# Kernel optimization log

Measured on AMD Instinct MI355X. Metric: run time of the kernel, lower is better.

## Reference

```python
import jax, jax.numpy as jnp
import numpy as np

B, H, W = 8, 64, 64
DIM1, DIM2 = 384, 256
NH, DH = 8, 32
INNER = NH * DH
EPS = 1e-5


def _layernorm(x, w, b):
    mu = jnp.mean(x, axis=-1, keepdims=True)
    var = jnp.mean((x - mu) ** 2, axis=-1, keepdims=True)
    return (x - mu) * jax.lax.rsqrt(var + EPS) * w + b


def _axial_attn(q, k, v, scale):
    # q,k,v: [B,H,W,nh,dh]; row attention over H, col attention over W
    sh = jnp.einsum('biwnd,bjwnd->bwnij', q, k) * scale  # [B,W,nh,H,H]
    oh = jnp.einsum('bwnij,bjwnd->biwnd', jax.nn.softmax(sh, axis=-1), v)
    sw = jnp.einsum('bhind,bhjnd->bhnij', q, k) * scale  # [B,H,nh,W,W]
    ow = jnp.einsum('bhnij,bhjnd->bhind', jax.nn.softmax(sw, axis=-1), v)
    return oh + ow  # [B,H,W,nh,dh]


def setup_inputs() -> dict:
    key = jax.random.key(0)
    ks = jax.random.split(key, 16)
    s1 = 1.0 / np.sqrt(DIM1)
    s2 = 1.0 / np.sqrt(DIM2)
    si = 1.0 / np.sqrt(INNER)
    return {
        'x1': jax.random.normal(ks[0], (B, DIM1, H, W), jnp.float32),
        'x2': jax.random.normal(ks[1], (B, DIM2, H, W), jnp.float32),
        'ln1q_w': jnp.ones((DIM1,), jnp.float32),
        'ln1q_b': jnp.zeros((DIM1,), jnp.float32),
        'ln2kv_w': jnp.ones((DIM2,), jnp.float32),
        'ln2kv_b': jnp.zeros((DIM2,), jnp.float32),
        'Wq1': jax.random.normal(ks[2], (DIM1, INNER), jnp.float32) * s1,
        'Wkv2': jax.random.normal(ks[3], (DIM2, 2 * INNER), jnp.float32) * s2,
        'Wout1': jax.random.normal(ks[4], (INNER, DIM2), jnp.float32) * si,
        'bout1': jnp.zeros((DIM2,), jnp.float32),
        'ln2q_w': jnp.ones((DIM2,), jnp.float32),
        'ln2q_b': jnp.zeros((DIM2,), jnp.float32),
        'ln1kv_w': jnp.ones((DIM1,), jnp.float32),
        'ln1kv_b': jnp.zeros((DIM1,), jnp.float32),
        'Wq2': jax.random.normal(ks[5], (DIM2, INNER), jnp.float32) * s2,
        'Wkv1': jax.random.normal(ks[6], (DIM1, 2 * INNER), jnp.float32) * s1,
        'Wout2': jax.random.normal(ks[7], (INNER, DIM2), jnp.float32) * si,
        'bout2': jnp.zeros((DIM2,), jnp.float32),
        'Wsc': jax.random.normal(ks[8], (DIM2, DIM1), jnp.float32) * s1,  # 1x1 conv [out,in]
        'bn_gamma': jnp.ones((DIM2,), jnp.float32),
        'bn_beta': jnp.zeros((DIM2,), jnp.float32),
        'bn_mean': jnp.zeros((DIM2,), jnp.float32),
        'bn_var': jnp.ones((DIM2,), jnp.float32),
    }


def reference(x1, x2, ln1q_w, ln1q_b, ln2kv_w, ln2kv_b, Wq1, Wkv2, Wout1, bout1,
              ln2q_w, ln2q_b, ln1kv_w, ln1kv_b, Wq2, Wkv1, Wout2, bout2,
              Wsc, bn_gamma, bn_beta, bn_mean, bn_var):
    b, c1, h, w = x1.shape
    scale = DH ** -0.5
    x1f = jnp.transpose(x1, (0, 2, 3, 1))  # [B,H,W,C1]
    x2f = jnp.transpose(x2, (0, 2, 3, 1))  # [B,H,W,C2]

    def heads(t):
        return t.reshape(b, h, w, NH, DH)

    # branch 1: q from x1, kv from x2
    q1 = _layernorm(x1f, ln1q_w, ln1q_b) @ Wq1
    kv2 = _layernorm(x2f, ln2kv_w, ln2kv_b) @ Wkv2
    k2, v2 = jnp.split(kv2, 2, axis=-1)
    o1 = _axial_attn(heads(q1), heads(k2), heads(v2), scale)
    fused1 = o1.reshape(b, h, w, INNER) @ Wout1 + bout1
    # shortcut: 1x1 conv + BN (inference stats)
    sc = jnp.einsum('bhwc,oc->bhwo', x1f, Wsc)
    sc = (sc - bn_mean) * jax.lax.rsqrt(bn_var + EPS) * bn_gamma + bn_beta
    y1 = sc + fused1

    # branch 2: q from x2, kv from x1
    q2 = _layernorm(x2f, ln2q_w, ln2q_b) @ Wq2
    kv1 = _layernorm(x1f, ln1kv_w, ln1kv_b) @ Wkv1
    k1, v1 = jnp.split(kv1, 2, axis=-1)
    o2 = _axial_attn(heads(q2), heads(k1), heads(v1), scale)
    fused2 = o2.reshape(b, h, w, INNER) @ Wout2 + bout2
    y2 = x2f + fused2

    out = y1 + y2  # [B,H,W,C2]
    return jnp.transpose(out, (0, 3, 1, 2))
```

## Files before the change

kernel.cpp:

```cpp
#include <hip/hip_runtime.h>

typedef unsigned short u16;
typedef unsigned int u32;
typedef float v4f __attribute__((ext_vector_type(4)));
typedef __bf16 v8bf __attribute__((ext_vector_type(8)));

__device__ __forceinline__ float bf2f(u16 v) {
  union { u32 u; float f; } x; x.u = ((u32)v) << 16; return x.f;
}
__device__ __forceinline__ u16 f2bf(float f) {
  union { float f; u32 u; } x; x.f = f;
  u32 u = x.u;
  return (u16)((u + 0x7FFFu + ((u >> 16) & 1u)) >> 16);
}

struct Ptrs { const void* p[23]; };

__global__ __launch_bounds__(256) void convert_all(Ptrs ps, u16* __restrict__ cx1,
                                                   u16* __restrict__ cx2,
                                                   u16* __restrict__ cw) {
  static const int sz[23]  = {12582912, 8388608, 384, 384, 256, 256, 98304, 131072,
                              65536, 256, 256, 256, 384, 384, 65536, 196608, 65536,
                              256, 98304, 256, 256, 256, 256};
  static const int off[23] = {0, 0, 0, 384, 768, 1024, 1280, 99584, 230656, 296192,
                              296448, 296704, 296960, 297344, 297728, 363264, 559872,
                              625408, 625664, 723968, 724224, 724480, 724736};
  const int ti = blockIdx.y;
  const int n8 = sz[ti] >> 3;
  const bool isf32 = (((const u32*)ps.p[2])[0] == 0x3F800000u);
  u16* dst = (ti == 0) ? cx1 : (ti == 1) ? cx2 : (cw + off[ti]);
  const void* src = ps.p[ti];
  const int stride = gridDim.x * blockDim.x;
  for (int i = blockIdx.x * blockDim.x + threadIdx.x; i < n8; i += stride) {
    if (isf32) {
      const float4 f0 = ((const float4*)src)[2*i];
      const float4 f1 = ((const float4*)src)[2*i + 1];
      u16 tmp[8];
      tmp[0] = f2bf(f0.x); tmp[1] = f2bf(f0.y); tmp[2] = f2bf(f0.z); tmp[3] = f2bf(f0.w);
      tmp[4] = f2bf(f1.x); tmp[5] = f2bf(f1.y); tmp[6] = f2bf(f1.z); tmp[7] = f2bf(f1.w);
      ((uint4*)dst)[i] = *(const uint4*)tmp;
    } else {
      ((uint4*)dst)[i] = ((const uint4*)src)[i];
    }
  }
}

__global__ void prep_bt(const u16* __restrict__ lnq_w, const u16* __restrict__ lnq_b,
                        const u16* __restrict__ lnkv_w, const u16* __restrict__ lnkv_b,
                        const u16* __restrict__ Wq, const u16* __restrict__ Wkv,
                        u16* __restrict__ BT, float* __restrict__ bias) {
  const int C = blockDim.x;
  const int j = blockIdx.x;
  const int c = threadIdx.x;
  float w, bco, wv;
  if (j < 256) { w = bf2f(lnq_w[c]); bco = bf2f(lnq_b[c]); wv = bf2f(Wq[c*256 + j]); }
  else         { w = bf2f(lnkv_w[c]); bco = bf2f(lnkv_b[c]); wv = bf2f(Wkv[c*512 + (j-256)]); }
  BT[(size_t)j*C + c] = f2bf(w * wv);
  __shared__ float red[384];
  red[c] = bco * wv;
  __syncthreads();
  if (c == 0) { float s = 0.f; for (int i = 0; i < C; i++) s += red[i]; bias[j] = s; }
}

__global__ void prep_fin(const u16* __restrict__ Wout1, const u16* __restrict__ Wout2,
                         const u16* __restrict__ Wsc, const u16* __restrict__ bout1,
                         const u16* __restrict__ bout2, const u16* __restrict__ gam,
                         const u16* __restrict__ bet, const u16* __restrict__ mean,
                         const u16* __restrict__ var, u16* __restrict__ BT,
                         float* __restrict__ bias) {
  const int o = blockIdx.x, t = threadIdx.x;
  const float g = rsqrtf(bf2f(var[o]) + 1e-5f) * bf2f(gam[o]);
  for (int idx = t; idx < 1408; idx += 256) {
    float v;
    if (idx < 512)       v = bf2f(Wout1[(idx & 255)*256 + o]);
    else if (idx < 1024) v = bf2f(Wout2[((idx - 512) & 255)*256 + o]);
    else                 v = bf2f(Wsc[o*384 + (idx - 1024)]) * g;
    BT[(size_t)o*1408 + idx] = f2bf(v);
  }
  if (t == 0) bias[o] = bf2f(bet[o]) - bf2f(mean[o])*g + bf2f(bout1[o]) + bf2f(bout2[o]);
}

__global__ __launch_bounds__(256) void ln_c384(const u16* __restrict__ x,
                                               u16* __restrict__ xn, u16* __restrict__ xraw) {
  __shared__ u16 tile[384*66];
  __shared__ float rsum[4][64], rsq[4][64], smean[64], srstd[64];
  const int t = threadIdx.x, w = t & 63, g = t >> 6;
  const int bh = blockIdx.x, b = bh >> 6, h = bh & 63;
  const u16* src = x + (size_t)b*384*4096 + h*64 + w;
  float sum = 0.f, sq = 0.f;
  for (int j = 0; j < 96; j++) {
    const int c = g*96 + j;
    const u16 uv = src[(size_t)c*4096];
    tile[c*66 + w] = uv;
    const float v = bf2f(uv); sum += v; sq += v*v;
  }
  rsum[g][w] = sum; rsq[g][w] = sq;
  __syncthreads();
  if (t < 64) {
    const float s = rsum[0][t]+rsum[1][t]+rsum[2][t]+rsum[3][t];
    const float q = rsq[0][t]+rsq[1][t]+rsq[2][t]+rsq[3][t];
    const float mean = s * (1.0f/384.0f);
    float var = q * (1.0f/384.0f) - mean*mean;
    if (var < 0.f) var = 0.f;
    smean[t] = mean; srstd[t] = rsqrtf(var + 1e-5f);
  }
  __syncthreads();
  const size_t pos0 = (size_t)bh * 64;
  for (int i = 0; i < 96; i++) {
    const int flat = i*256 + t;
    const int ww = flat / 384, c = flat - ww*384;
    const u16 uv = tile[c*66 + ww];
    const float v = (bf2f(uv) - smean[ww]) * srstd[ww];
    const size_t p = pos0 + ww;
    xn[p*384 + c] = f2bf(v);
    xraw[p*384 + c] = uv;
  }
}

__global__ __launch_bounds__(256) void ln_c256(const u16* __restrict__ x,
                                               u16* __restrict__ xn) {
  __shared__ u16 tile[256*66];
  __shared__ float rsum[4][64], rsq[4][64], smean[64], srstd[64];
  const int t = threadIdx.x, w = t & 63, g = t >> 6;
  const int bh = blockIdx.x, b = bh >> 6, h = bh & 63;
  const u16* src = x + (size_t)b*256*4096 + h*64 + w;
  float sum = 0.f, sq = 0.f;
  for (int j = 0; j < 64; j++) {
    const int c = g*64 + j;
    const u16 uv = src[(size_t)c*4096];
    tile[c*66 + w] = uv;
    const float v = bf2f(uv); sum += v; sq += v*v;
  }
  rsum[g][w] = sum; rsq[g][w] = sq;
  __syncthreads();
  if (t < 64) {
    const float s = rsum[0][t]+rsum[1][t]+rsum[2][t]+rsum[3][t];
    const float q = rsq[0][t]+rsq[1][t]+rsq[2][t]+rsq[3][t];
    const float mean = s * (1.0f/256.0f);
    float var = q * (1.0f/256.0f) - mean*mean;
    if (var < 0.f) var = 0.f;
    smean[t] = mean; srstd[t] = rsqrtf(var + 1e-5f);
  }
  __syncthreads();
  const size_t pos0 = (size_t)bh * 64;
  for (int i = 0; i < 64; i++) {
    const int flat = i*256 + t;
    const int ww = flat >> 8, c = flat & 255;
    const float v = (bf2f(tile[c*66 + ww]) - smean[ww]) * srstd[ww];
    xn[(pos0 + ww)*256 + c] = f2bf(v);
  }
}

__global__ __launch_bounds__(256) void gemm_bt(const u16* __restrict__ A,
                                               const u16* __restrict__ BT,
                                               u16* __restrict__ C,
                                               const float* __restrict__ bias,
                                               int N, int K) {
  __shared__ u16 lsA[128*40];
  __shared__ u16 lsB[128*40];
  const int t = threadIdx.x;
  const int m0 = blockIdx.x * 128, n0 = blockIdx.y * 128;
  const int lane = t & 63, wv = t >> 6;
  const int wm = wv & 1, wn = wv >> 1;
  const int lo = lane & 15, hi = lane >> 4;
  const int r0 = t >> 2, c8 = (t & 3) << 3;
  const u16* Ab = A + (size_t)(m0 + r0) * K + c8;
  const u16* Bb = BT + (size_t)(n0 + r0) * K + c8;
  v4f acc[4][4] = {};
  for (int kb = 0; kb < K; kb += 32) {
    uint4 a0 = *(const uint4*)(Ab + kb);
    uint4 a1 = *(const uint4*)(Ab + (size_t)64*K + kb);
    uint4 b0 = *(const uint4*)(Bb + kb);
    uint4 b1 = *(const uint4*)(Bb + (size_t)64*K + kb);
    __syncthreads();
    *(uint4*)&lsA[r0*40 + c8] = a0;
    *(uint4*)&lsA[(r0+64)*40 + c8] = a1;
    *(uint4*)&lsB[r0*40 + c8] = b0;
    *(uint4*)&lsB[(r0+64)*40 + c8] = b1;
    __syncthreads();
    v8bf av[4], bv[4];
#pragma unroll
    for (int i = 0; i < 4; i++) av[i] = *(const v8bf*)&lsA[(wm*64 + i*16 + lo)*40 + hi*8];
#pragma unroll
    for (int i = 0; i < 4; i++) bv[i] = *(const v8bf*)&lsB[(wn*64 + i*16 + lo)*40 + hi*8];
#pragma unroll
    for (int mt = 0; mt < 4; mt++)
#pragma unroll
      for (int nt = 0; nt < 4; nt++)
        acc[mt][nt] = __builtin_amdgcn_mfma_f32_16x16x32_bf16(av[mt], bv[nt], acc[mt][nt], 0, 0, 0);
  }
#pragma unroll
  for (int mt = 0; mt < 4; mt++) {
    const int row = m0 + wm*64 + mt*16 + hi*4;
#pragma unroll
    for (int nt = 0; nt < 4; nt++) {
      const int col = n0 + wn*64 + nt*16 + lo;
      const float bs = bias[col];
#pragma unroll
      for (int r = 0; r < 4; r++)
        C[(size_t)(row + r) * N + col] = f2bf(acc[mt][nt][r] + bs);
    }
  }
}

__global__ __launch_bounds__(256) void gemm_final(const u16* __restrict__ Ao,
                                                  const u16* __restrict__ Ar,
                                                  const u16* __restrict__ BT,
                                                  const float* __restrict__ bias,
                                                  const u16* __restrict__ x2c,
                                                  const u32* __restrict__ probe,
                                                  void* __restrict__ outv) {
  __shared__ u16 smem[16640];
  u16* lsA = smem;
  u16* lsB = smem + 5120;
  const int t = threadIdx.x;
  const int m0 = blockIdx.x * 128, n0 = blockIdx.y * 128;
  const int lane = t & 63, wv = t >> 6;
  const int wm = wv & 1, wn = wv >> 1;
  const int lo = lane & 15, hi = lane >> 4;
  const int r0 = t >> 2, c8 = (t & 3) << 3;
  const u16* AoR = Ao + (size_t)(m0 + r0) * 1024 + c8;
  const u16* ArR = Ar + (size_t)(m0 + r0) * 384 + c8;
  const u16* Bb  = BT + (size_t)(n0 + r0) * 1408 + c8;
  v4f acc[4][4] = {};
  for (int kb = 0; kb < 1408; kb += 32) {
    uint4 a0, a1;
    if (kb < 1024) { a0 = *(const uint4*)(AoR + kb); a1 = *(const uint4*)(AoR + 64*1024 + kb); }
    else { a0 = *(const uint4*)(ArR + (kb-1024)); a1 = *(const uint4*)(ArR + 64*384 + (kb-1024)); }
    uint4 b0 = *(const uint4*)(Bb + kb);
    uint4 b1 = *(const uint4*)(Bb + 64*1408 + kb);
    __syncthreads();
    *(uint4*)&lsA[r0*40 + c8] = a0;
    *(uint4*)&lsA[(r0+64)*40 + c8] = a1;
    *(uint4*)&lsB[r0*40 + c8] = b0;
    *(uint4*)&lsB[(r0+64)*40 + c8] = b1;
    __syncthreads();
    v8bf av[4], bv[4];
#pragma unroll
    for (int i = 0; i < 4; i++) av[i] = *(const v8bf*)&lsA[(wm*64 + i*16 + lo)*40 + hi*8];
#pragma unroll
    for (int i = 0; i < 4; i++) bv[i] = *(const v8bf*)&lsB[(wn*64 + i*16 + lo)*40 + hi*8];
#pragma unroll
    for (int mt = 0; mt < 4; mt++)
#pragma unroll
      for (int nt = 0; nt < 4; nt++)
        acc[mt][nt] = __builtin_amdgcn_mfma_f32_16x16x32_bf16(av[mt], bv[nt], acc[mt][nt], 0, 0, 0);
  }
  __syncthreads();
#pragma unroll
  for (int mt = 0; mt < 4; mt++)
#pragma unroll
    for (int nt = 0; nt < 4; nt++) {
      const int nl = wn*64 + nt*16 + lo;
      const float bs = bias[n0 + nl];
#pragma unroll
      for (int r = 0; r < 4; r++)
        smem[(wm*64 + mt*16 + hi*4 + r)*130 + nl] = f2bf(acc[mt][nt][r] + bs);
    }
  __syncthreads();
  const bool isf32 = (probe[0] == 0x3F800000u);
  const int bh0 = blockIdx.x * 2;
  for (int i = 0; i < 64; i++) {
    const int flat = i*256 + t;
    const int nl = flat >> 7;
    const int rem = flat & 127;
    const int mb = rem >> 6, w = rem & 63;
    const int bh = bh0 + mb, b = bh >> 6, h = bh & 63;
    const size_t oidx = ((size_t)(b*256 + n0 + nl)*64 + h)*64 + w;
    const float val = bf2f(smem[(mb*64 + w)*130 + nl]) + bf2f(x2c[oidx]);
    if (isf32) ((float*)outv)[oidx] = val;
    else       ((u16*)outv)[oidx]   = f2bf(val);
  }
}

__global__ __launch_bounds__(64) void attn(const u16* __restrict__ qkv1,
                                           const u16* __restrict__ qkv2,
                                           u16* __restrict__ Ao) {
  __shared__ u16 lq[64*40], lk[64*40];
  __shared__ u16 lvt[32*72];
  __shared__ u16 lp[64*72];
  const int t = threadIdx.x;
  const int lo = t & 15, hi = t >> 4;
  const int bx = blockIdx.x;
  const int head = blockIdx.y;
  const int z = blockIdx.z;
  const int br = z >> 1, dir = z & 1;
  const int b = bx >> 6, x = bx & 63;
  const u16* Qb  = (br == 0) ? qkv1 : qkv2;
  const u16* KVb = (br == 0) ? qkv2 : qkv1;
  const int qc = head*32, kc = 256 + head*32, vc = 512 + head*32;
  const int pbase = (dir == 0) ? (b*4096 + x) : ((b*64 + x)*64);
  const int pstr  = (dir == 0) ? 64 : 1;
  {
    const size_t p = (size_t)(pbase + t*pstr) * 768;
    const u16* qr = Qb + p + qc;
    const u16* kr = KVb + p + kc;
    const u16* vr = KVb + p + vc;
    *(uint4*)&lq[t*40+ 0] = *(const uint4*)(qr+ 0);
    *(uint4*)&lq[t*40+ 8] = *(const uint4*)(qr+ 8);
    *(uint4*)&lq[t*40+16] = *(const uint4*)(qr+16);
    *(uint4*)&lq[t*40+24] = *(const uint4*)(qr+24);
    *(uint4*)&lk[t*40+ 0] = *(const uint4*)(kr+ 0);
    *(uint4*)&lk[t*40+ 8] = *(const uint4*)(kr+ 8);
    *(uint4*)&lk[t*40+16] = *(const uint4*)(kr+16);
    *(uint4*)&lk[t*40+24] = *(const uint4*)(kr+24);
    u16 vbuf[32];
    *(uint4*)&vbuf[ 0] = *(const uint4*)(vr+ 0);
    *(uint4*)&vbuf[ 8] = *(const uint4*)(vr+ 8);
    *(uint4*)&vbuf[16] = *(const uint4*)(vr+16);
    *(uint4*)&vbuf[24] = *(const uint4*)(vr+24);
#pragma unroll
    for (int d = 0; d < 32; d++) lvt[d*72 + t] = vbuf[d];
  }
  __syncthreads();
  v4f s[4][4];
  {
    v8bf qa[4], ka[4];
#pragma unroll
    for (int i = 0; i < 4; i++) qa[i] = *(const v8bf*)&lq[(i*16 + lo)*40 + hi*8];
#pragma unroll
    for (int i = 0; i < 4; i++) ka[i] = *(const v8bf*)&lk[(i*16 + lo)*40 + hi*8];
#pragma unroll
    for (int mt = 0; mt < 4; mt++)
#pragma unroll
      for (int nt = 0; nt < 4; nt++) {
        v4f z4 = {};
        s[mt][nt] = __builtin_amdgcn_mfma_f32_16x16x32_bf16(qa[mt], ka[nt], z4, 0, 0, 0);
      }
  }
  const float scale = 0.17677669529663687f;
#pragma unroll
  for (int mt = 0; mt < 4; mt++)
#pragma unroll
    for (int r = 0; r < 4; r++) {
      float v0 = s[mt][0][r]*scale, v1 = s[mt][1][r]*scale;
      float v2 = s[mt][2][r]*scale, v3 = s[mt][3][r]*scale;
      float mx = fmaxf(fmaxf(v0, v1), fmaxf(v2, v3));
#pragma unroll
      for (int off = 1; off < 16; off <<= 1) mx = fmaxf(mx, __shfl_xor(mx, off));
      float e0 = __expf(v0 - mx), e1 = __expf(v1 - mx);
      float e2 = __expf(v2 - mx), e3 = __expf(v3 - mx);
      float sm = e0 + e1 + e2 + e3;
#pragma unroll
      for (int off = 1; off < 16; off <<= 1) sm += __shfl_xor(sm, off);
      const float inv = 1.0f / sm;
      const int row = mt*16 + hi*4 + r;
      lp[row*72 +  0 + lo] = f2bf(e0*inv);
      lp[row*72 + 16 + lo] = f2bf(e1*inv);
      lp[row*72 + 32 + lo] = f2bf(e2*inv);
      lp[row*72 + 48 + lo] = f2bf(e3*inv);
    }
  __syncthreads();
  v4f o[4][2] = {};
#pragma unroll
  for (int ks = 0; ks < 2; ks++) {
    v8bf pa[4], vb[2];
#pragma unroll
    for (int i = 0; i < 4; i++) pa[i] = *(const v8bf*)&lp[(i*16 + lo)*72 + ks*32 + hi*8];
#pragma unroll
    for (int i = 0; i < 2; i++) vb[i] = *(const v8bf*)&lvt[(i*16 + lo)*72 + ks*32 + hi*8];
#pragma unroll
    for (int mt = 0; mt < 4; mt++)
#pragma unroll
      for (int nt = 0; nt < 2; nt++)
        o[mt][nt] = __builtin_amdgcn_mfma_f32_16x16x32_bf16(pa[mt], vb[nt], o[mt][nt], 0, 0, 0);
  }
  const int oc = z*256 + head*32;
#pragma unroll
  for (int mt = 0; mt < 4; mt++)
#pragma unroll
    for (int r = 0; r < 4; r++) {
      const int i = mt*16 + hi*4 + r;
      const size_t pv = (size_t)(pbase + i*pstr) * 1024 + oc;
      Ao[pv + lo]      = f2bf(o[mt][0][r]);
      Ao[pv + 16 + lo] = f2bf(o[mt][1][r]);
    }
}

extern "C" void kernel_launch(void* const* d_in, const int* in_sizes, int n_in,
                              void* d_out, int out_size, void* d_ws, size_t ws_size,
                              hipStream_t stream) {
  char* ws = (char*)d_ws;
  u16* Ao    = (u16*)(ws);
  u16* Araw  = (u16*)(ws + 67108864);
  u16* qkv1  = (u16*)(ws + 92274688);
  u16* qkv2  = (u16*)(ws + 142606336);
  u16* cx2   = (u16*)(ws + 192937984);
  u16* cw    = (u16*)(ws + 209715200);
  u16* BT1   = (u16*)(ws + 211165184);
  u16* BT2   = (u16*)(ws + 211755008);
  u16* BTf   = (u16*)(ws + 212148224);
  float* bias1 = (float*)(ws + 212869120);
  float* bias2 = (float*)(ws + 212872192);
  float* biasf = (float*)(ws + 212875264);
  u16* cx1 = qkv1;
  u16* x1n = Ao;
  u16* x2n = Ao + 12582912;

  u16* c_ln1q_w = cw + 0,     *c_ln1q_b = cw + 384;
  u16* c_ln2kv_w = cw + 768,  *c_ln2kv_b = cw + 1024;
  u16* c_Wq1 = cw + 1280,     *c_Wkv2 = cw + 99584;
  u16* c_Wout1 = cw + 230656, *c_bout1 = cw + 296192;
  u16* c_ln2q_w = cw + 296448,*c_ln2q_b = cw + 296704;
  u16* c_ln1kv_w = cw + 296960,*c_ln1kv_b = cw + 297344;
  u16* c_Wq2 = cw + 297728,   *c_Wkv1 = cw + 363264;
  u16* c_Wout2 = cw + 559872, *c_bout2 = cw + 625408;
  u16* c_Wsc = cw + 625664;
  u16* c_bn_g = cw + 723968,  *c_bn_b = cw + 724224;
  u16* c_bn_m = cw + 724480,  *c_bn_v = cw + 724736;

  Ptrs ps;
  for (int i = 0; i < 23; i++) ps.p[i] = d_in[i];

  convert_all<<<dim3(512, 23), 256, 0, stream>>>(ps, cx1, cx2, cw);
  prep_bt<<<768, 384, 0, stream>>>(c_ln1q_w, c_ln1q_b, c_ln1kv_w, c_ln1kv_b, c_Wq1, c_Wkv1, BT1, bias1);
  prep_bt<<<768, 256, 0, stream>>>(c_ln2q_w, c_ln2q_b, c_ln2kv_w, c_ln2kv_b, c_Wq2, c_Wkv2, BT2, bias2);
  prep_fin<<<256, 256, 0, stream>>>(c_Wout1, c_Wout2, c_Wsc, c_bout1, c_bout2,
                                    c_bn_g, c_bn_b, c_bn_m, c_bn_v, BTf, biasf);
  ln_c384<<<512, 256, 0, stream>>>(cx1, x1n, Araw);
  ln_c256<<<512, 256, 0, stream>>>(cx2, x2n);
  gemm_bt<<<dim3(256, 6), 256, 0, stream>>>(x1n, BT1, qkv1, bias1, 768, 384);
  gemm_bt<<<dim3(256, 6), 256, 0, stream>>>(x2n, BT2, qkv2, bias2, 768, 256);
  attn<<<dim3(512, 8, 4), 64, 0, stream>>>(qkv1, qkv2, Ao);
  gemm_final<<<dim3(256, 2), 256, 0, stream>>>(Ao, Araw, BTf, biasf, cx2,
                                               (const u32*)d_in[2], d_out);
}
```

Measured before the change: 406.3 us.

## Transpose attention MFMA operands so softmax and output stores are row-contiguous

The attention kernel swaps the MFMA operand order so each lane holds a column of scores for one query. The softmax then reduces mostly in registers with only two cross-lane shuffles. Probabilities and outputs are packed two bf16 at a time into 32-bit LDS writes using round-half-up truncation. Outputs are staged through shared memory and written to global as 16-byte vector stores instead of scattered 2-byte stores. Shared buffers are merged into one aliased array, which adds extra barriers and changes rounding slightly.

```diff
diff --git a/kernel.cpp b/kernel.cpp
--- a/kernel.cpp
+++ b/kernel.cpp
@@ -12,6 +12,14 @@
   union { float f; u32 u; } x; x.f = f;
   u32 u = x.u;
   return (u16)((u + 0x7FFFu + ((u >> 16) & 1u)) >> 16);
+}
+__device__ __forceinline__ u32 f2u(float f) {
+  union { float f; u32 u; } x; x.f = f; return x.u;
+}
+__device__ __forceinline__ u32 pk2bf(float a, float b) {
+  const u32 au = f2u(a) + 0x8000u;
+  const u32 bu = f2u(b) + 0x8000u;
+  return (bu & 0xFFFF0000u) | (au >> 16);
 }
 
 struct Ptrs { const void* p[23]; };
@@ -276,11 +284,10 @@
 __global__ __launch_bounds__(64) void attn(const u16* __restrict__ qkv1,
                                            const u16* __restrict__ qkv2,
                                            u16* __restrict__ Ao) {
-  __shared__ u16 lq[64*40], lk[64*40];
-  __shared__ u16 lvt[32*72];
-  __shared__ u16 lp[64*72];
+  __shared__ u16 smem[7424];
+  constexpr int LVT = 0, LQ = 2304, LK = 4864, LP = 2304, LO = 2304;
   const int t = threadIdx.x;
-  const int lo = t & 15, hi = t >> 4;
+  const int lo = t & 15, quad = t >> 4;
   const int bx = blockIdx.x;
   const int head = blockIdx.y;
   const int z = blockIdx.z;
@@ -296,85 +303,103 @@
     const u16* qr = Qb + p + qc;
     const u16* kr = KVb + p + kc;
     const u16* vr = KVb + p + vc;
-    *(uint4*)&lq[t*40+ 0] = *(const uint4*)(qr+ 0);
-    *(uint4*)&lq[t*40+ 8] = *(const uint4*)(qr+ 8);
-    *(uint4*)&lq[t*40+16] = *(const uint4*)(qr+16);
-    *(uint4*)&lq[t*40+24] = *(const uint4*)(qr+24);
-    *(uint4*)&lk[t*40+ 0] = *(const uint4*)(kr+ 0);
-    *(uint4*)&lk[t*40+ 8] = *(const uint4*)(kr+ 8);
-    *(uint4*)&lk[t*40+16] = *(const uint4*)(kr+16);
-    *(uint4*)&lk[t*40+24] = *(const uint4*)(kr+24);
+#pragma unroll
+    for (int i = 0; i < 4; i++) *(uint4*)&smem[LQ + t*40 + i*8] = *(const uint4*)(qr + i*8);
+#pragma unroll
+    for (int i = 0; i < 4; i++) *(uint4*)&smem[LK + t*40 + i*8] = *(const uint4*)(kr + i*8);
     u16 vbuf[32];
-    *(uint4*)&vbuf[ 0] = *(const uint4*)(vr+ 0);
-    *(uint4*)&vbuf[ 8] = *(const uint4*)(vr+ 8);
-    *(uint4*)&vbuf[16] = *(const uint4*)(vr+16);
-    *(uint4*)&vbuf[24] = *(const uint4*)(vr+24);
-#pragma unroll
-    for (int d = 0; d < 32; d++) lvt[d*72 + t] = vbuf[d];
+#pragma unroll
+    for (int i = 0; i < 4; i++) *(uint4*)&vbuf[i*8] = *(const uint4*)(vr + i*8);
+#pragma unroll
+    for (int d = 0; d < 32; d++) smem[LVT + d*72 + t] = vbuf[d];
   }
   __syncthreads();
   v4f s[4][4];
   {
     v8bf qa[4], ka[4];
 #pragma unroll
-    for (int i = 0; i < 4; i++) qa[i] = *(const v8bf*)&lq[(i*16 + lo)*40 + hi*8];
-#pragma unroll
-    for (int i = 0; i < 4; i++) ka[i] = *(const v8bf*)&lk[(i*16 + lo)*40 + hi*8];
-#pragma unroll
-    for (int mt = 0; mt < 4; mt++)
+    for (int i = 0; i < 4; i++) qa[i] = *(const v8bf*)&smem[LQ + (i*16 + lo)*40 + quad*8];
+#pragma unroll
+    for (int i = 0; i < 4; i++) ka[i] = *(const v8bf*)&smem[LK + (i*16 + lo)*40 + quad*8];
+#pragma unroll
+    for (int qt = 0; qt < 4; qt++)
+#pragma unroll
+      for (int kt = 0; kt < 4; kt++) {
+        v4f z4 = {};
+        s[qt][kt] = __builtin_amdgcn_mfma_f32_16x16x32_bf16(ka[kt], qa[qt], z4, 0, 0, 0);
+      }
+  }
+  __syncthreads();
+  const float scale = 0.17677669529663687f;
+#pragma unroll
+  for (int qt = 0; qt < 4; qt++) {
+    float tv[16];
+    float mx = -1e30f;
+#pragma unroll
+    for (int kt = 0; kt < 4; kt++)
+#pragma unroll
+      for (int r = 0; r < 4; r++) {
+        const float v = s[qt][kt][r] * scale;
+        tv[kt*4 + r] = v;
+        mx = fmaxf(mx, v);
+      }
+    mx = fmaxf(mx, __shfl_xor(mx, 16));
+    mx = fmaxf(mx, __shfl_xor(mx, 32));
+    float sm = 0.f;
+#pragma unroll
+    for (int i = 0; i < 16; i++) { tv[i] = __expf(tv[i] - mx); sm += tv[i]; }
+    sm += __shfl_xor(sm, 16);
+    sm += __shfl_xor(sm, 32);
+    const float inv = 1.0f / sm;
+    const int q = qt*16 + lo;
+#pragma unroll
+    for (int kt = 0; kt < 4; kt++)
+#pragma unroll
+      for (int rp = 0; rp < 2; rp++) {
+        const u32 pk = pk2bf(tv[kt*4 + rp*2] * inv, tv[kt*4 + rp*2 + 1] * inv);
+        *(u32*)&smem[LP + q*72 + kt*16 + quad*4 + rp*2] = pk;
+      }
+  }
+  __syncthreads();
+  v4f o[2][4] = {};
+  {
+    v8bf va[2][2], pb[4][2];
+#pragma unroll
+    for (int mt = 0; mt < 2; mt++)
+#pragma unroll
+      for (int ks = 0; ks < 2; ks++)
+        va[mt][ks] = *(const v8bf*)&smem[LVT + (mt*16 + lo)*72 + ks*32 + quad*8];
+#pragma unroll
+    for (int nt = 0; nt < 4; nt++)
+#pragma unroll
+      for (int ks = 0; ks < 2; ks++)
+        pb[nt][ks] = *(const v8bf*)&smem[LP + (nt*16 + lo)*72 + ks*32 + quad*8];
+#pragma unroll
+    for (int mt = 0; mt < 2; mt++)
 #pragma unroll
       for (int nt = 0; nt < 4; nt++) {
-        v4f z4 = {};
-        s[mt][nt] = __builtin_amdgcn_mfma_f32_16x16x32_bf16(qa[mt], ka[nt], z4, 0, 0, 0);
+        o[mt][nt] = __builtin_amdgcn_mfma_f32_16x16x32_bf16(va[mt][0], pb[nt][0], o[mt][nt], 0, 0, 0);
+        o[mt][nt] = __builtin_amdgcn_mfma_f32_16x16x32_bf16(va[mt][1], pb[nt][1], o[mt][nt], 0, 0, 0);
       }
   }
-  const float scale = 0.17677669529663687f;
-#pragma unroll
-  for (int mt = 0; mt < 4; mt++)
-#pragma unroll
-    for (int r = 0; r < 4; r++) {
-      float v0 = s[mt][0][r]*scale, v1 = s[mt][1][r]*scale;
-      float v2 = s[mt][2][r]*scale, v3 = s[mt][3][r]*scale;
-      float mx = fmaxf(fmaxf(v0, v1), fmaxf(v2, v3));
-#pragma unroll
-      for (int off = 1; off < 16; off <<= 1) mx = fmaxf(mx, __shfl_xor(mx, off));
-      float e0 = __expf(v0 - mx), e1 = __expf(v1 - mx);
-      float e2 = __expf(v2 - mx), e3 = __expf(v3 - mx);
-      float sm = e0 + e1 + e2 + e3;
-#pragma unroll
-      for (int off = 1; off < 16; off <<= 1) sm += __shfl_xor(sm, off);
-      const float inv = 1.0f / sm;
-      const int row = mt*16 + hi*4 + r;
-      lp[row*72 +  0 + lo] = f2bf(e0*inv);
-      lp[row*72 + 16 + lo] = f2bf(e1*inv);
-      lp[row*72 + 32 + lo] = f2bf(e2*inv);
-      lp[row*72 + 48 + lo] = f2bf(e3*inv);
-    }
-  __syncthreads();
-  v4f o[4][2] = {};
-#pragma unroll
-  for (int ks = 0; ks < 2; ks++) {
-    v8bf pa[4], vb[2];
-#pragma unroll
-    for (int i = 0; i < 4; i++) pa[i] = *(const v8bf*)&lp[(i*16 + lo)*72 + ks*32 + hi*8];
-#pragma unroll
-    for (int i = 0; i < 2; i++) vb[i] = *(const v8bf*)&lvt[(i*16 + lo)*72 + ks*32 + hi*8];
-#pragma unroll
-    for (int mt = 0; mt < 4; mt++)
-#pragma unroll
-      for (int nt = 0; nt < 2; nt++)
-        o[mt][nt] = __builtin_amdgcn_mfma_f32_16x16x32_bf16(pa[mt], vb[nt], o[mt][nt], 0, 0, 0);
-  }
-  const int oc = z*256 + head*32;
-#pragma unroll
-  for (int mt = 0; mt < 4; mt++)
-#pragma unroll
-    for (int r = 0; r < 4; r++) {
-      const int i = mt*16 + hi*4 + r;
-      const size_t pv = (size_t)(pbase + i*pstr) * 1024 + oc;
-      Ao[pv + lo]      = f2bf(o[mt][0][r]);
-      Ao[pv + 16 + lo] = f2bf(o[mt][1][r]);
-    }
+  __syncthreads();
+#pragma unroll
+  for (int mt = 0; mt < 2; mt++)
+#pragma unroll
+    for (int nt = 0; nt < 4; nt++)
+#pragma unroll
+      for (int rp = 0; rp < 2; rp++) {
+        const u32 pk = pk2bf(o[mt][nt][rp*2], o[mt][nt][rp*2 + 1]);
+        *(u32*)&smem[LO + (nt*16 + lo)*40 + mt*16 + quad*4 + rp*2] = pk;
+      }
+  __syncthreads();
+  {
+    const int oc = z*256 + head*32;
+    const size_t gbase = (size_t)(pbase + t*pstr) * 1024 + oc;
+#pragma unroll
+    for (int i = 0; i < 4; i++)
+      *(uint4*)&Ao[gbase + i*8] = *(const uint4*)&smem[LO + t*40 + i*8];
+  }
 }
 
 extern "C" void kernel_launch(void* const* d_in, const int* in_sizes, int n_in,
```

Measured after the change: 380.6 us. -6.3%, faster.
